# Performance work log

Measured on AMD Instinct MI355X. Metric: run time of the kernel, lower is better.

Reference implementation:

```python
import jax, jax.numpy as jnp
import numpy as np

N_USER = 100000
M_ITEM = 50000
N_NODE = N_USER + M_ITEM
D = 64           # latent_dim
WD = D // 2      # word_emb_dim
FU = FI = 10     # padded feature-bag width
NUF = NIF = 30000
VOCAB = 20000
T = 8            # tokens per text source (name/comment/comment_list)
DNU = DNI = 10   # numeric feature dims
B = 2048         # seed batch
S = 20           # sampled neighbors per layer
L = 2            # num_layers


def setup_inputs() -> dict:
    key = jax.random.key(0)
    ks = jax.random.split(key, 26)
    f = lambda i, s: jax.random.normal(ks[i], s, jnp.float32) * 0.05
    ri = lambda i, s, hi: jax.random.randint(ks[i], s, 0, hi)
    return {
        # int (graph / lookup) inputs
        "seeds": ri(0, (B,), N_USER),
        "neigh1": ri(1, (B, S), N_NODE),
        "neigh2": ri(2, (B, S, S), N_NODE),
        "user_feat_idx": ri(3, (N_USER, FU), NUF),
        "item_feat_idx": ri(4, (M_ITEM, FI), NIF),
        "user_text_idx": ri(5, (N_USER, 3, T), VOCAB),
        "item_text_idx": ri(6, (M_ITEM, 3, T), VOCAB),
        # float tables / features
        "user_id_emb": f(7, (N_USER, D)),
        "item_id_emb": f(8, (M_ITEM, D)),
        "user_feat_emb": f(9, (NUF, D)),
        "item_feat_emb": f(10, (NIF, D)),
        "word_emb": f(11, (VOCAB, WD)),
        "user_word300": f(12, (N_USER, 300)),
        "item_word300": f(13, (M_ITEM, 300)),
        "item_sent768": f(14, (M_ITEM, 768)),
        "user_numeric": f(15, (N_USER, DNU)),
        "item_numeric": f(16, (M_ITEM, DNI)),
        # linears (stored as (in, out); y = x @ W + b)
        "Wnum_u": f(17, (DNU, D)), "bnum_u": jnp.zeros((D,), jnp.float32),
        "Wnum_i": f(18, (DNI, D)), "bnum_i": jnp.zeros((D,), jnp.float32),
        "Wproj_u": f(19, (int(D * 3.5) + 300, D)), "bproj_u": jnp.zeros((D,), jnp.float32),
        "Wproj_i": f(20, (int(D * 3.5) + 300 + 768, D)), "bproj_i": jnp.zeros((D,), jnp.float32),
        "W_w": f(21, (L, 2 * D, D)), "b_w": jnp.zeros((L, D), jnp.float32),
        "W_v": f(22, (L, D, D)), "b_v": jnp.zeros((L, D), jnp.float32),
    }


def _forward(user_id_emb, item_id_emb, user_feat_emb, item_feat_emb, word_emb,
             user_word300, item_word300, item_sent768, user_numeric, item_numeric,
             Wnum_u, bnum_u, Wnum_i, bnum_i, Wproj_u, bproj_u, Wproj_i, bproj_i,
             W_w, b_w, W_v, b_v,
             seeds, neigh1, neigh2, user_feat_idx, item_feat_idx,
             user_text_idx, item_text_idx):
    # --- multi-source node embeddings (get_text_embedding + proj + numeric) ---
    # text: mean-pool word embeddings per source, concat 3 sources -> 1.5*D
    u_text = word_emb[user_text_idx].mean(axis=2).reshape(N_USER, 3 * WD)
    i_text = word_emb[item_text_idx].mean(axis=2).reshape(M_ITEM, 3 * WD)
    # feature bags: mean-pooled embedding lookup
    u_feat = user_feat_emb[user_feat_idx].mean(axis=1)
    i_feat = item_feat_emb[item_feat_idx].mean(axis=1)
    u = (jnp.concatenate([user_id_emb, u_feat, u_text, user_word300], -1) @ Wproj_u
         + bproj_u + user_numeric @ Wnum_u + bnum_u)
    it = (jnp.concatenate([item_id_emb, i_feat, i_text, item_word300, item_sent768], -1) @ Wproj_i
          + bproj_i + item_numeric @ Wnum_i + bnum_i)
    x = jnp.concatenate([u, it], axis=0)  # [N_NODE, D], items offset by N_USER

    # --- neighbor-sampled GraphSAGE: h = W_l([self, mean(V_l(neigh))]) ---
    def sage(l, self_x, neigh_x, act):
        agg = (neigh_x @ W_v[l] + b_v[l]).mean(axis=-2)
        h = jnp.concatenate([self_x, agg], axis=-1) @ W_w[l] + b_w[l]
        return jax.nn.relu(h) if act else h

    x0 = x[seeds]        # [B, D]
    x1 = x[neigh1]       # [B, S, D]
    x2 = x[neigh2]       # [B, S, S, D]
    h1 = sage(0, x1, x2, True)   # layer-0 applied to 1-hop nodes
    h0 = sage(0, x0, x1, True)   # layer-0 applied to seeds
    out = sage(1, h0, h1, False)  # final layer, no activation
    return out  # [B, D]


def reference(seeds, neigh1, neigh2, user_feat_idx, item_feat_idx, user_text_idx,
              item_text_idx, user_id_emb, item_id_emb, user_feat_emb, item_feat_emb,
              word_emb, user_word300, item_word300, item_sent768, user_numeric,
              item_numeric, Wnum_u, bnum_u, Wnum_i, bnum_i, Wproj_u, bproj_u,
              Wproj_i, bproj_i, W_w, b_w, W_v, b_v):
    return _forward(user_id_emb, item_id_emb, user_feat_emb, item_feat_emb, word_emb,
                    user_word300, item_word300, item_sent768, user_numeric, item_numeric,
                    Wnum_u, bnum_u, Wnum_i, bnum_i, Wproj_u, bproj_u, Wproj_i, bproj_i,
                    W_w, b_w, W_v, b_v,
                    seeds, neigh1, neigh2, user_feat_idx, item_feat_idx,
                    user_text_idx, item_text_idx)
```

## Files before the change

kernel.cpp:

```cpp
#include <hip/hip_runtime.h>
#include <hip/hip_bf16.h>
#include <stdint.h>

#define N_USER 100000
#define M_ITEM 50000
#define N_NODE 150000
#define B_SEED 2048
#define S_NB 20
#define UBLK2 1563
#define IBLK2 782

typedef __bf16   bf16x8 __attribute__((ext_vector_type(8)));
typedef float    f32x4  __attribute__((ext_vector_type(4)));
typedef uint32_t u32x4  __attribute__((ext_vector_type(4)));

typedef __attribute__((address_space(3))) uint32_t lds_u32_t;
typedef __attribute__((address_space(1))) const uint32_t glb_u32_t;

__device__ __forceinline__ uint16_t f2bf(float f) {
    uint32_t u = __float_as_uint(f);
    return (uint16_t)((u + 0x7FFFu + ((u >> 16) & 1u)) >> 16);
}
__device__ __forceinline__ uint32_t pk2(float a, float b) {
    __hip_bfloat162 h = __float22bfloat162_rn(make_float2(a, b));
    return *reinterpret_cast<uint32_t*>(&h);
}
__device__ __forceinline__ float bf2f(uint16_t u) {
    return __uint_as_float(((uint32_t)u) << 16);
}

union BF8 { bf16x8 v; uint32_t u[4]; };

__device__ __forceinline__ bf16x8 pack8v(f32x4 lo, f32x4 hi) {
    BF8 r;
    r.u[0] = pk2(lo[0], lo[1]); r.u[1] = pk2(lo[2], lo[3]);
    r.u[2] = pk2(hi[0], hi[1]); r.u[3] = pk2(hi[2], hi[3]);
    return r.v;
}
__device__ __forceinline__ bf16x8 ldf32x8_mask(const float* rowp, int base, int limit) {
    BF8 r;
#pragma unroll
    for (int h = 0; h < 4; ++h) {
        const int k0 = base + 2 * h;
        const float a = (k0     < limit) ? rowp[k0]     : 0.f;
        const float b = (k0 + 1 < limit) ? rowp[k0 + 1] : 0.f;
        r.u[h] = pk2(a, b);
    }
    return r.v;
}

__global__ void prep_kernel(const float* __restrict__ Wproj_u, const float* __restrict__ Wnum_u,
                            const float* __restrict__ Wproj_i, const float* __restrict__ Wnum_i,
                            const float* __restrict__ Wv0, const float* __restrict__ Ww0,
                            uint16_t* __restrict__ WTU, uint16_t* __restrict__ WTI,
                            uint16_t* __restrict__ WvT, uint16_t* __restrict__ WwT)
{
    const int idx = blockIdx.x * 256 + threadIdx.x;
    if (idx < 36864) {
        const int d = idx / 576, kp = idx - d * 576;
        float v = 0.f;
        if (kp < 160)      v = Wproj_u[(64 + kp) * 64 + d];
        else if (kp < 192) { const int j = kp - 160; if (j < 10) v = Wnum_u[j * 64 + d]; }
        else if (kp < 224) { const int j = kp - 192; if (j < 12) v = Wproj_u[(512 + j) * 64 + d]; }
        else if (kp < 288) v = Wproj_u[(kp - 224) * 64 + d];
        else               v = Wproj_u[(224 + kp - 288) * 64 + d];
        WTU[d * 576 + kp] = f2bf(v);
    } else if (idx < 122880) {
        const int i2 = idx - 36864;
        const int d = i2 / 1344, kp = i2 - d * 1344;
        float v = 0.f;
        if (kp < 160)      v = Wproj_i[(64 + kp) * 64 + d];
        else if (kp < 192) { const int j = kp - 160; if (j < 10) v = Wnum_i[j * 64 + d]; }
        else if (kp < 224) { const int j = kp - 192; if (j < 12) v = Wproj_i[(512 + j) * 64 + d]; }
        else if (kp < 288) v = Wproj_i[(kp - 224) * 64 + d];
        else if (kp < 576) v = Wproj_i[(224 + kp - 288) * 64 + d];
        else               v = Wproj_i[(524 + kp - 576) * 64 + d];
        WTI[d * 1344 + kp] = f2bf(v);
    } else {
        const int i2 = idx - 122880;
        if (i2 < 4096) { const int d = i2 >> 6, k = i2 & 63;  WvT[d * 64 + k]  = f2bf(Wv0[k * 64 + d]); }
        else           { const int j = i2 - 4096;
                         const int d = j >> 7, k = j & 127;   WwT[d * 128 + k] = f2bf(Ww0[k * 64 + d]); }
    }
}

__global__ __launch_bounds__(256) void gpack_kernel(
    const int* __restrict__ ufi, const int* __restrict__ ifi,
    const int* __restrict__ uti, const int* __restrict__ iti,
    const float* __restrict__ ufe, const float* __restrict__ ife,
    const float* __restrict__ wemb,
    uint16_t* __restrict__ Apre)
{
    const int gid  = blockIdx.x * 256 + threadIdx.x;
    const int node = gid >> 3;
    const int d0   = gid & 7;
    if (node >= N_NODE) return;
    const bool item = node >= N_USER;
    const int nloc  = item ? node - N_USER : node;
    const int*   fidx = (item ? ifi : ufi) + (size_t)nloc * 10;
    const int*   tidx = (item ? iti : uti) + (size_t)nloc * 24;
    const float* fe   = item ? ife : ufe;
    uint16_t* out = Apre + (size_t)node * 160;

    {
        f32x4 s0 = {0, 0, 0, 0}, s1 = {0, 0, 0, 0};
#pragma unroll
        for (int j = 0; j < 10; ++j) {
            const float* p = fe + (size_t)fidx[j] * 64 + 8 * d0;
            s0 += *(const f32x4*)p;
            s1 += *(const f32x4*)(p + 4);
        }
        s0 *= 0.1f; s1 *= 0.1f;
        uint4 o = make_uint4(pk2(s0[0], s0[1]), pk2(s0[2], s0[3]),
                             pk2(s1[0], s1[1]), pk2(s1[2], s1[3]));
        *(uint4*)(out + 8 * d0) = o;
    }
#pragma unroll
    for (int s = 0; s < 3; ++s) {
        f32x4 a = {0, 0, 0, 0};
#pragma unroll
        for (int j = 0; j < 8; ++j) {
            const float* p = wemb + (size_t)tidx[s * 8 + j] * 32 + 4 * d0;
            a += *(const f32x4*)p;
        }
        a *= 0.125f;
        *(uint2*)(out + 64 + 32 * s + 4 * d0) = make_uint2(pk2(a[0], a[1]), pk2(a[2], a[3]));
    }
}

__global__ __launch_bounds__(256, 6) void pgemm_kernel(
    const uint16_t* __restrict__ Apre,
    const float* __restrict__ u_id,  const float* __restrict__ i_id,
    const float* __restrict__ uw300, const float* __restrict__ iw300,
    const float* __restrict__ is768,
    const float* __restrict__ unum,  const float* __restrict__ inum,
    const uint16_t* __restrict__ WTU, const uint16_t* __restrict__ WTI,
    const float* __restrict__ bproj_u, const float* __restrict__ bnum_u,
    const float* __restrict__ bproj_i, const float* __restrict__ bnum_i,
    uint16_t* __restrict__ xout)
{
    __shared__ float buf[2][2048];

    const int t = threadIdx.x;
    const int w = t >> 6, l = t & 63;
    const int l15 = l & 15, g4 = l >> 4;
    const bool item = blockIdx.x < IBLK2;
    const int tile  = item ? blockIdx.x : (blockIdx.x - IBLK2);
    const int ntype = item ? M_ITEM : N_USER;
    const int nb    = tile * 64;
    const int NC    = item ? 35 : 11;

    const float* idp = item ? i_id  : u_id;
    const float* w3p = item ? iw300 : uw300;
    const float* nmp = item ? inum  : unum;
    const uint16_t* WT = item ? WTI : WTU;
    const int KP       = item ? 1344 : 576;

    f32x4 acc[4] = {};
    const uint16_t* WTb = WT + (size_t)l15 * KP + g4 * 8;

    auto MM = [&](bf16x8 af, int kb) {
#pragma unroll
        for (int db = 0; db < 4; ++db) {
            const bf16x8 bfr = *reinterpret_cast<const bf16x8*>(WTb + (size_t)db * 16 * KP + kb);
            acc[db] = __builtin_amdgcn_mfma_f32_16x16x32_bf16(af, bfr, acc[db], 0, 0, 0);
        }
    };

    auto stage = [&](int bi, int c) {
        const float* base; int stride, coloff;
        if (c < 2)       { base = idp;    stride = 64;  coloff = c * 32; }
        else if (c < 11) { base = w3p;    stride = 300; coloff = (c - 2) * 32; }
        else             { base = is768;  stride = 768; coloff = (c - 11) * 32; }
#pragma unroll
        for (int j = 0; j < 2; ++j) {
            const int row  = w * 16 + j * 8 + (l >> 3);
            const int node = (nb + row) < ntype ? (nb + row) : (ntype - 1);
            const int swb  = ((l & 7) * 16) ^ ((row & 7) << 4);
            const float* g = base + (size_t)node * stride + coloff + (swb >> 2);
            uint32_t* lp = (uint32_t*)((char*)&buf[bi][0] + w * 2048 + j * 1024);
            __builtin_amdgcn_global_load_lds((glb_u32_t*)g, (lds_u32_t*)lp, 16, 0, 0);
        }
    };

    auto compute = [&](int bi, int kb) {
        const char* bb = (const char*)&buf[bi][0];
        const int r = w * 16 + l15;
        const f32x4 lo = *(const f32x4*)(bb + r * 128 + ((g4 * 32)      ^ ((r & 7) << 4)));
        const f32x4 hi = *(const f32x4*)(bb + r * 128 + ((g4 * 32 + 16) ^ ((r & 7) << 4)));
        MM(pack8v(lo, hi), kb);
    };

    stage(0, 0);
    {
        const int nloc = (nb + w * 16 + l15) < ntype ? (nb + w * 16 + l15) : (ntype - 1);
        const int node = (item ? N_USER : 0) + nloc;
        const uint16_t* ap = Apre + (size_t)node * 160 + g4 * 8;
        bf16x8 af[5];
#pragma unroll
        for (int ks = 0; ks < 5; ++ks) af[ks] = *(const bf16x8*)(ap + ks * 32);
#pragma unroll
        for (int ks = 0; ks < 5; ++ks) MM(af[ks], ks * 32);
        MM(ldf32x8_mask(nmp + (size_t)nloc * 10, g4 * 8, 10), 160);
        MM(ldf32x8_mask(w3p + (size_t)nloc * 300, 288 + g4 * 8, 300), 192);
    }

    for (int c = 0; c < NC; ++c) {
        if (c + 1 < NC) stage((c + 1) & 1, c + 1);
        __syncthreads();
        compute(c & 1, 224 + 32 * c);
        __syncthreads();
    }

    const int nb_out = nb + w * 16 + g4 * 4;
    const float* bp = item ? bproj_i : bproj_u;
    const float* bn = item ? bnum_i  : bnum_u;
    uint16_t* xo = xout + (size_t)(item ? N_USER : 0) * 64;
#pragma unroll
    for (int db = 0; db < 4; ++db) {
        const int d = db * 16 + l15;
        const float bias = bp[d] + bn[d];
#pragma unroll
        for (int r = 0; r < 4; ++r) {
            const int nn = nb_out + r;
            if (nn < ntype) xo[(size_t)nn * 64 + d] = f2bf(acc[db][r] + bias);
        }
    }
}

__global__ __launch_bounds__(256) void xv_kernel(
    const uint16_t* __restrict__ x, const uint16_t* __restrict__ WvT,
    const float* __restrict__ bv, uint16_t* __restrict__ xv, int n)
{
    const int t = threadIdx.x;
    const int w = t >> 6, l = t & 63, l15 = l & 15, g4 = l >> 4;
    const int node = blockIdx.x * 64 + w * 16 + l15;
    const int node_c = node < n ? node : n - 1;

    f32x4 acc[4] = {};
    const uint16_t* WTb = WvT + l15 * 64 + g4 * 8;
#pragma unroll
    for (int ks = 0; ks < 2; ++ks) {
        const bf16x8 af = *reinterpret_cast<const bf16x8*>(x + (size_t)node_c * 64 + ks * 32 + g4 * 8);
#pragma unroll
        for (int db = 0; db < 4; ++db) {
            const bf16x8 bfr = *reinterpret_cast<const bf16x8*>(WTb + db * 16 * 64 + ks * 32);
            acc[db] = __builtin_amdgcn_mfma_f32_16x16x32_bf16(af, bfr, acc[db], 0, 0, 0);
        }
    }
    const int node_base = blockIdx.x * 64 + w * 16 + g4 * 4;
#pragma unroll
    for (int db = 0; db < 4; ++db) {
        const int d = db * 16 + l15;
        const float bias = bv[d];
#pragma unroll
        for (int r = 0; r < 4; ++r) {
            const int nn = node_base + r;
            if (nn < n) xv[(size_t)nn * 64 + d] = f2bf(acc[db][r] + bias);
        }
    }
}

__global__ __launch_bounds__(256) void sage_mfma_kernel(
    const uint16_t* __restrict__ x, const uint16_t* __restrict__ xv,
    const int* __restrict__ self_idx, const int* __restrict__ neigh_idx,
    const uint16_t* __restrict__ WwT, const float* __restrict__ bw,
    uint16_t* __restrict__ out, int relu)
{
    const int t = threadIdx.x;
    const int w = t >> 6, l = t & 63, l15 = l & 15, g4 = l >> 4;
    const int r = blockIdx.x * 64 + w * 16 + l15;
    const int sidx = self_idx[r];
    const int* ni = neigh_idx + (size_t)r * S_NB;

    f32x4 acc[4] = {};
    const uint16_t* WTb = WwT + l15 * 128 + g4 * 8;

    auto MM = [&](bf16x8 af, int kb) {
#pragma unroll
        for (int db = 0; db < 4; ++db) {
            const bf16x8 bfr = *reinterpret_cast<const bf16x8*>(WTb + db * 16 * 128 + kb);
            acc[db] = __builtin_amdgcn_mfma_f32_16x16x32_bf16(af, bfr, acc[db], 0, 0, 0);
        }
    };

#pragma unroll
    for (int ks = 0; ks < 2; ++ks) {
        const bf16x8 af = *reinterpret_cast<const bf16x8*>(x + (size_t)sidx * 64 + ks * 32 + g4 * 8);
        MM(af, ks * 32);
    }
#pragma unroll
    for (int ks = 0; ks < 2; ++ks) {
        float ev[4] = {0.f, 0.f, 0.f, 0.f}, od[4] = {0.f, 0.f, 0.f, 0.f};
#pragma unroll
        for (int j = 0; j < S_NB; ++j) {
            const u32x4 v = *reinterpret_cast<const u32x4*>(xv + (size_t)ni[j] * 64 + ks * 32 + g4 * 8);
#pragma unroll
            for (int q = 0; q < 4; ++q) {
                ev[q] += __uint_as_float(v[q] << 16);
                od[q] += __uint_as_float(v[q] & 0xffff0000u);
            }
        }
        BF8 m;
#pragma unroll
        for (int q = 0; q < 4; ++q) m.u[q] = pk2(ev[q] * (1.f / S_NB), od[q] * (1.f / S_NB));
        MM(m.v, 64 + ks * 32);
    }

    const int rb = blockIdx.x * 64 + w * 16 + g4 * 4;
#pragma unroll
    for (int db = 0; db < 4; ++db) {
        const int d = db * 16 + l15;
        const float bias = bw[d];
#pragma unroll
        for (int rr = 0; rr < 4; ++rr) {
            float h = acc[db][rr] + bias;
            if (relu) h = fmaxf(h, 0.f);
            out[(size_t)(rb + rr) * 64 + d] = f2bf(h);
        }
    }
}

__global__ __launch_bounds__(256) void final_kernel(
    const uint16_t* __restrict__ h0, const uint16_t* __restrict__ h1,
    const float* __restrict__ Wv, const float* __restrict__ bv,
    const float* __restrict__ Ww, const float* __restrict__ bw,
    float* __restrict__ out)
{
    __shared__ float WvL[64 * 64];
    __shared__ float WwL[128 * 64];
    const int t = threadIdx.x;
    for (int i = t; i < 64 * 64; i += 256)  WvL[i] = Wv[i];
    for (int i = t; i < 128 * 64; i += 256) WwL[i] = Ww[i];
    __syncthreads();

    const int wave = t >> 6, lane = t & 63;
    const int base = blockIdx.x * 32 + wave * 8;
    const float bvl = bv[lane], bwl = bw[lane];

    for (int i = 0; i < 8; ++i) {
        const int b = base + i;
        float m = 0.f;
#pragma unroll
        for (int s = 0; s < S_NB; ++s)
            m += bf2f(h1[(size_t)(b * S_NB + s) * 64 + lane]);
        m *= (1.f / S_NB);

        float agg = bvl;
#pragma unroll 8
        for (int k = 0; k < 64; ++k)
            agg += __shfl(m, k) * WvL[k * 64 + lane];

        const float selfv = bf2f(h0[(size_t)b * 64 + lane]);
        float h = bwl;
#pragma unroll 8
        for (int k = 0; k < 64; ++k)
            h += __shfl(selfv, k) * WwL[k * 64 + lane];
#pragma unroll 8
        for (int k = 0; k < 64; ++k)
            h += __shfl(agg, k) * WwL[(64 + k) * 64 + lane];

        out[(size_t)b * 64 + lane] = h;
    }
}

extern "C" void kernel_launch(void* const* d_in, const int* in_sizes, int n_in,
                              void* d_out, int out_size, void* d_ws, size_t ws_size,
                              hipStream_t stream)
{
    const int*   seeds   = (const int*)d_in[0];
    const int*   neigh1  = (const int*)d_in[1];
    const int*   neigh2  = (const int*)d_in[2];
    const int*   ufi     = (const int*)d_in[3];
    const int*   ifi     = (const int*)d_in[4];
    const int*   uti     = (const int*)d_in[5];
    const int*   iti     = (const int*)d_in[6];
    const float* u_id    = (const float*)d_in[7];
    const float* i_id    = (const float*)d_in[8];
    const float* ufe     = (const float*)d_in[9];
    const float* ife     = (const float*)d_in[10];
    const float* wemb    = (const float*)d_in[11];
    const float* uw300   = (const float*)d_in[12];
    const float* iw300   = (const float*)d_in[13];
    const float* is768   = (const float*)d_in[14];
    const float* unum    = (const float*)d_in[15];
    const float* inum    = (const float*)d_in[16];
    const float* Wnum_u  = (const float*)d_in[17];
    const float* bnum_u  = (const float*)d_in[18];
    const float* Wnum_i  = (const float*)d_in[19];
    const float* bnum_i  = (const float*)d_in[20];
    const float* Wproj_u = (const float*)d_in[21];
    const float* bproj_u = (const float*)d_in[22];
    const float* Wproj_i = (const float*)d_in[23];
    const float* bproj_i = (const float*)d_in[24];
    const float* W_w     = (const float*)d_in[25];
    const float* b_w     = (const float*)d_in[26];
    const float* W_v     = (const float*)d_in[27];
    const float* b_v     = (const float*)d_in[28];

    uint16_t* WTU  = (uint16_t*)d_ws;
    uint16_t* WTI  = WTU  + 36864;
    uint16_t* WvT0 = WTI  + 86016;
    uint16_t* WwT0 = WvT0 + 4096;
    uint16_t* xbf  = WwT0 + 8192;
    uint16_t* xvbf = xbf  + (size_t)N_NODE * 64;
    uint16_t* h1bf = xvbf + (size_t)N_NODE * 64;
    uint16_t* h0bf = h1bf + (size_t)B_SEED * S_NB * 64;
    uint16_t* Apre = xvbf;
    float* outp = (float*)d_out;

    prep_kernel<<<528, 256, 0, stream>>>(
        Wproj_u, Wnum_u, Wproj_i, Wnum_i, W_v, W_w, WTU, WTI, WvT0, WwT0);

    gpack_kernel<<<(N_NODE * 8 + 255) / 256, 256, 0, stream>>>(
        ufi, ifi, uti, iti, ufe, ife, wemb, Apre);

    pgemm_kernel<<<UBLK2 + IBLK2, 256, 0, stream>>>(
        Apre, u_id, i_id, uw300, iw300, is768, unum, inum,
        WTU, WTI, bproj_u, bnum_u, bproj_i, bnum_i, xbf);

    xv_kernel<<<(N_NODE + 63) / 64, 256, 0, stream>>>(xbf, WvT0, b_v, xvbf, N_NODE);

    sage_mfma_kernel<<<(B_SEED * S_NB) / 64, 256, 0, stream>>>(
        xbf, xvbf, neigh1, neigh2, WwT0, b_w, h1bf, 1);
    sage_mfma_kernel<<<B_SEED / 64, 256, 0, stream>>>(
        xbf, xvbf, seeds, neigh1, WwT0, b_w, h0bf, 1);

    final_kernel<<<B_SEED / 32, 256, 0, stream>>>(
        h0bf, h1bf, W_v + 4096, b_v + 64, W_w + 8192, b_w + 64, outp);
}
```

Measured before the change: 337.3 us.

## Deepen pgemm LDS pipeline to four stages with vmcnt waits instead of barriers

Replaces the double-buffered LDS staging in the projection GEMM with a four-slot ring. Each wave waits only on its own outstanding global-to-LDS loads via s_waitcnt vmcnt, which works because every wave stages and reads only its own rows, so the two __syncthreads per chunk go away. The prologue loads of the precomputed features are now issued alongside the first prefetches so their latency overlaps. In exchange, LDS use per block doubles and the occupancy hint in launch_bounds is removed, which may lower the number of resident blocks.

Measured after the change: 353.0 us. 4.6% more time.

```diff
diff --git a/kernel.cpp b/kernel.cpp
--- a/kernel.cpp
+++ b/kernel.cpp
@@ -9,6 +9,7 @@
 #define S_NB 20
 #define UBLK2 1563
 #define IBLK2 782
+#define DEPTH 4
 
 typedef __bf16   bf16x8 __attribute__((ext_vector_type(8)));
 typedef float    f32x4  __attribute__((ext_vector_type(4)));
@@ -47,6 +48,11 @@
         r.u[h] = pk2(a, b);
     }
     return r.v;
+}
+
+template<int N> __device__ __forceinline__ void waitcnt_vm() {
+    asm volatile("s_waitcnt vmcnt(%0)" :: "n"(N) : "memory");
+    __builtin_amdgcn_sched_barrier(0);
 }
 
 __global__ void prep_kernel(const float* __restrict__ Wproj_u, const float* __restrict__ Wnum_u,
@@ -128,7 +134,7 @@
     }
 }
 
-__global__ __launch_bounds__(256, 6) void pgemm_kernel(
+__global__ __launch_bounds__(256) void pgemm_kernel(
     const uint16_t* __restrict__ Apre,
     const float* __restrict__ u_id,  const float* __restrict__ i_id,
     const float* __restrict__ uw300, const float* __restrict__ iw300,
@@ -139,7 +145,7 @@
     const float* __restrict__ bproj_i, const float* __restrict__ bnum_i,
     uint16_t* __restrict__ xout)
 {
-    __shared__ float buf[2][2048];
+    __shared__ float buf[DEPTH][2048];
 
     const int t = threadIdx.x;
     const int w = t >> 6, l = t & 63;
@@ -191,26 +197,32 @@
         MM(pack8v(lo, hi), kb);
     };
 
-    stage(0, 0);
-    {
-        const int nloc = (nb + w * 16 + l15) < ntype ? (nb + w * 16 + l15) : (ntype - 1);
-        const int node = (item ? N_USER : 0) + nloc;
-        const uint16_t* ap = Apre + (size_t)node * 160 + g4 * 8;
-        bf16x8 af[5];
-#pragma unroll
-        for (int ks = 0; ks < 5; ++ks) af[ks] = *(const bf16x8*)(ap + ks * 32);
-#pragma unroll
-        for (int ks = 0; ks < 5; ++ks) MM(af[ks], ks * 32);
-        MM(ldf32x8_mask(nmp + (size_t)nloc * 10, g4 * 8, 10), 160);
-        MM(ldf32x8_mask(w3p + (size_t)nloc * 300, 288 + g4 * 8, 300), 192);
-    }
-
-    for (int c = 0; c < NC; ++c) {
-        if (c + 1 < NC) stage((c + 1) & 1, c + 1);
-        __syncthreads();
-        compute(c & 1, 224 + 32 * c);
-        __syncthreads();
-    }
+    const int nloc = (nb + w * 16 + l15) < ntype ? (nb + w * 16 + l15) : (ntype - 1);
+    const int node = (item ? N_USER : 0) + nloc;
+    const uint16_t* ap = Apre + (size_t)node * 160 + g4 * 8;
+    bf16x8 af[5];
+#pragma unroll
+    for (int ks = 0; ks < 5; ++ks) af[ks] = *(const bf16x8*)(ap + ks * 32);
+    const bf16x8 numf  = ldf32x8_mask(nmp + (size_t)nloc * 10, g4 * 8, 10);
+    const bf16x8 tailf = ldf32x8_mask(w3p + (size_t)nloc * 300, 288 + g4 * 8, 300);
+
+#pragma unroll
+    for (int d = 0; d < DEPTH - 1; ++d) stage(d, d);
+
+#pragma unroll
+    for (int ks = 0; ks < 5; ++ks) MM(af[ks], ks * 32);
+    MM(numf, 160);
+    MM(tailf, 192);
+
+#pragma unroll 1
+    for (int c = 0; c < NC - (DEPTH - 1); ++c) {
+        stage((c + DEPTH - 1) & (DEPTH - 1), c + DEPTH - 1);
+        waitcnt_vm<2 * (DEPTH - 1)>();
+        compute(c & (DEPTH - 1), 224 + 32 * c);
+    }
+    waitcnt_vm<4>(); compute((NC - 3) & (DEPTH - 1), 224 + 32 * (NC - 3));
+    waitcnt_vm<2>(); compute((NC - 2) & (DEPTH - 1), 224 + 32 * (NC - 2));
+    waitcnt_vm<0>(); compute((NC - 1) & (DEPTH - 1), 224 + 32 * (NC - 1));
 
     const int nb_out = nb + w * 16 + g4 * 4;
     const float* bp = item ? bproj_i : bproj_u;
```

## Double pgemm staging chunk width and fuse both layer-0 SAGE launches

Applied to the files above, without the earlier changes.

The projection GEMM now stages 64-column chunks (16 KB per buffer) instead of 32-column ones, which halves the number of barrier-separated stage/compute iterations. The leftover 300-wide columns are loaded directly from global memory, and the 1344/576 K layout is remapped to match. The two layer-0 SAGE launches (1-hop nodes and seeds) are merged into one 672-block launch that selects its index arrays per wave. The larger LDS footprint may lower occupancy under the 6-blocks-per-CU launch bound, and the direct global loads add some uncoalesced traffic.

Result: no change. 340.2 us (+0.9%).

```diff
diff --git a/kernel.cpp b/kernel.cpp
--- a/kernel.cpp
+++ b/kernel.cpp
@@ -139,7 +139,7 @@
     const float* __restrict__ bproj_i, const float* __restrict__ bnum_i,
     uint16_t* __restrict__ xout)
 {
-    __shared__ float buf[2][2048];
+    __shared__ float buf[2][4096];
 
     const int t = threadIdx.x;
     const int w = t >> 6, l = t & 63;
@@ -148,7 +148,7 @@
     const int tile  = item ? blockIdx.x : (blockIdx.x - IBLK2);
     const int ntype = item ? M_ITEM : N_USER;
     const int nb    = tile * 64;
-    const int NC    = item ? 35 : 11;
+    const int NC    = item ? 17 : 5;
 
     const float* idp = item ? i_id  : u_id;
     const float* w3p = item ? iw300 : uw300;
@@ -159,56 +159,66 @@
     f32x4 acc[4] = {};
     const uint16_t* WTb = WT + (size_t)l15 * KP + g4 * 8;
 
-    auto MM = [&](bf16x8 af, int kb) {
+    auto MM = [&](bf16x8 af2, int kb) {
 #pragma unroll
         for (int db = 0; db < 4; ++db) {
             const bf16x8 bfr = *reinterpret_cast<const bf16x8*>(WTb + (size_t)db * 16 * KP + kb);
-            acc[db] = __builtin_amdgcn_mfma_f32_16x16x32_bf16(af, bfr, acc[db], 0, 0, 0);
+            acc[db] = __builtin_amdgcn_mfma_f32_16x16x32_bf16(af2, bfr, acc[db], 0, 0, 0);
         }
     };
 
     auto stage = [&](int bi, int c) {
         const float* base; int stride, coloff;
-        if (c < 2)       { base = idp;    stride = 64;  coloff = c * 32; }
-        else if (c < 11) { base = w3p;    stride = 300; coloff = (c - 2) * 32; }
-        else             { base = is768;  stride = 768; coloff = (c - 11) * 32; }
-#pragma unroll
-        for (int j = 0; j < 2; ++j) {
-            const int row  = w * 16 + j * 8 + (l >> 3);
-            const int node = (nb + row) < ntype ? (nb + row) : (ntype - 1);
-            const int swb  = ((l & 7) * 16) ^ ((row & 7) << 4);
+        if (c == 0)      { base = idp;   stride = 64;  coloff = 0; }
+        else if (c < 5)  { base = w3p;   stride = 300; coloff = (c - 1) * 64; }
+        else             { base = is768; stride = 768; coloff = (c - 5) * 64; }
+        char* wbase = (char*)&buf[bi][0] + w * 4096;
+#pragma unroll
+        for (int j = 0; j < 4; ++j) {
+            const int row  = j * 4 + (l >> 4);
+            const int nn   = nb + w * 16 + row;
+            const int node = nn < ntype ? nn : (ntype - 1);
+            const int swb  = ((l & 15) * 16) ^ ((row & 7) << 4);
             const float* g = base + (size_t)node * stride + coloff + (swb >> 2);
-            uint32_t* lp = (uint32_t*)((char*)&buf[bi][0] + w * 2048 + j * 1024);
-            __builtin_amdgcn_global_load_lds((glb_u32_t*)g, (lds_u32_t*)lp, 16, 0, 0);
+            __builtin_amdgcn_global_load_lds((glb_u32_t*)g,
+                (lds_u32_t*)(void*)(wbase + j * 1024), 16, 0, 0);
         }
     };
 
-    auto compute = [&](int bi, int kb) {
-        const char* bb = (const char*)&buf[bi][0];
-        const int r = w * 16 + l15;
-        const f32x4 lo = *(const f32x4*)(bb + r * 128 + ((g4 * 32)      ^ ((r & 7) << 4)));
-        const f32x4 hi = *(const f32x4*)(bb + r * 128 + ((g4 * 32 + 16) ^ ((r & 7) << 4)));
-        MM(pack8v(lo, hi), kb);
+    auto compute = [&](int bi, int kb0) {
+        const char* wbase = (const char*)&buf[bi][0] + w * 4096;
+        const int r = l15;
+#pragma unroll
+        for (int ks = 0; ks < 2; ++ks) {
+            const f32x4 lo = *(const f32x4*)(wbase + r * 256 + ((ks * 128 + g4 * 32)      ^ ((r & 7) << 4)));
+            const f32x4 hi = *(const f32x4*)(wbase + r * 256 + ((ks * 128 + g4 * 32 + 16) ^ ((r & 7) << 4)));
+            MM(pack8v(lo, hi), kb0 + ks * 32);
+        }
     };
 
+    const int nloc = (nb + w * 16 + l15) < ntype ? (nb + w * 16 + l15) : (ntype - 1);
+    const int node = (item ? N_USER : 0) + nloc;
+    const uint16_t* ap = Apre + (size_t)node * 160 + g4 * 8;
+    bf16x8 af[5];
+#pragma unroll
+    for (int ks = 0; ks < 5; ++ks) af[ks] = *(const bf16x8*)(ap + ks * 32);
+    const float* wr = w3p + (size_t)nloc * 300;
+    const bf16x8 numf  = ldf32x8_mask(nmp + (size_t)nloc * 10, g4 * 8, 10);
+    const bf16x8 tailf = ldf32x8_mask(wr, 288 + g4 * 8, 300);
+    const bf16x8 w300c = pack8v(*(const f32x4*)(wr + 256 + g4 * 8),
+                                *(const f32x4*)(wr + 260 + g4 * 8));
+
     stage(0, 0);
-    {
-        const int nloc = (nb + w * 16 + l15) < ntype ? (nb + w * 16 + l15) : (ntype - 1);
-        const int node = (item ? N_USER : 0) + nloc;
-        const uint16_t* ap = Apre + (size_t)node * 160 + g4 * 8;
-        bf16x8 af[5];
-#pragma unroll
-        for (int ks = 0; ks < 5; ++ks) af[ks] = *(const bf16x8*)(ap + ks * 32);
-#pragma unroll
-        for (int ks = 0; ks < 5; ++ks) MM(af[ks], ks * 32);
-        MM(ldf32x8_mask(nmp + (size_t)nloc * 10, g4 * 8, 10), 160);
-        MM(ldf32x8_mask(w3p + (size_t)nloc * 300, 288 + g4 * 8, 300), 192);
-    }
+#pragma unroll
+    for (int ks = 0; ks < 5; ++ks) MM(af[ks], ks * 32);
+    MM(numf, 160);
+    MM(tailf, 192);
+    MM(w300c, 544);
 
     for (int c = 0; c < NC; ++c) {
         if (c + 1 < NC) stage((c + 1) & 1, c + 1);
         __syncthreads();
-        compute(c & 1, 224 + 32 * c);
+        compute(c & 1, (c < 5) ? 224 + 64 * c : 576 + 64 * (c - 5));
         __syncthreads();
     }
 
@@ -261,17 +271,21 @@
     }
 }
 
-__global__ __launch_bounds__(256) void sage_mfma_kernel(
+__global__ __launch_bounds__(256) void sage_fused_kernel(
     const uint16_t* __restrict__ x, const uint16_t* __restrict__ xv,
-    const int* __restrict__ self_idx, const int* __restrict__ neigh_idx,
+    const int* __restrict__ seeds, const int* __restrict__ neigh1,
+    const int* __restrict__ neigh2,
     const uint16_t* __restrict__ WwT, const float* __restrict__ bw,
-    uint16_t* __restrict__ out, int relu)
+    uint16_t* __restrict__ h1, uint16_t* __restrict__ h0)
 {
     const int t = threadIdx.x;
     const int w = t >> 6, l = t & 63, l15 = l & 15, g4 = l >> 4;
-    const int r = blockIdx.x * 64 + w * 16 + l15;
-    const int sidx = self_idx[r];
-    const int* ni = neigh_idx + (size_t)r * S_NB;
+    const int rbase = blockIdx.x * 64 + w * 16;
+    const bool is1 = rbase < 40960;
+    const int r = rbase + l15;
+    const int sidx = is1 ? neigh1[r] : seeds[r - 40960];
+    const int* ni = is1 ? (neigh2 + (size_t)r * S_NB)
+                        : (neigh1 + (size_t)(r - 40960) * S_NB);
 
     f32x4 acc[4] = {};
     const uint16_t* WTb = WwT + l15 * 128 + g4 * 8;
@@ -308,15 +322,16 @@
     }
 
     const int rb = blockIdx.x * 64 + w * 16 + g4 * 4;
+    uint16_t* ob = is1 ? h1 : h0;
+    const int rowoff = is1 ? 0 : 40960;
 #pragma unroll
     for (int db = 0; db < 4; ++db) {
         const int d = db * 16 + l15;
         const float bias = bw[d];
 #pragma unroll
         for (int rr = 0; rr < 4; ++rr) {
-            float h = acc[db][rr] + bias;
-            if (relu) h = fmaxf(h, 0.f);
-            out[(size_t)(rb + rr) * 64 + d] = f2bf(h);
+            const float h = fmaxf(acc[db][rr] + bias, 0.f);
+            ob[(size_t)(rb + rr - rowoff) * 64 + d] = f2bf(h);
         }
     }
 }
@@ -421,10 +436,8 @@
 
     xv_kernel<<<(N_NODE + 63) / 64, 256, 0, stream>>>(xbf, WvT0, b_v, xvbf, N_NODE);
 
-    sage_mfma_kernel<<<(B_SEED * S_NB) / 64, 256, 0, stream>>>(
-        xbf, xvbf, neigh1, neigh2, WwT0, b_w, h1bf, 1);
-    sage_mfma_kernel<<<B_SEED / 64, 256, 0, stream>>>(
-        xbf, xvbf, seeds, neigh1, WwT0, b_w, h0bf, 1);
+    sage_fused_kernel<<<672, 256, 0, stream>>>(
+        xbf, xvbf, seeds, neigh1, neigh2, WwT0, b_w, h1bf, h0bf);
 
     final_kernel<<<B_SEED / 32, 256, 0, stream>>>(
         h0bf, h1bf, W_v + 4096, b_v + 64, W_w + 8192, b_w + 64, outp);
```
